# Kernel optimization log

Measured on AMD Instinct MI355X. Metric: run time of the kernel, lower is better.

Reference implementation:

```python
import jax, jax.numpy as jnp
import numpy as np
import math

NUM_HEADS = 16
NUM_BUCKETS = 32
MAX_DISTANCE = 128


def _relative_position_bucket(relative_position, num_buckets=NUM_BUCKETS, max_distance=MAX_DISTANCE):
    num_buckets = num_buckets // 2
    ret = (relative_position >= 0).astype(jnp.int32) * num_buckets
    n = jnp.abs(relative_position)
    max_exact = num_buckets // 2
    is_small = n < max_exact
    # guard log(0); masked by is_small anyway
    n_safe = jnp.maximum(n, 1).astype(jnp.float32)
    val_if_large = max_exact + (
        jnp.log(n_safe / max_exact) / math.log(max_distance / max_exact) * (num_buckets - max_exact)
    ).astype(jnp.int32)
    val_if_large = jnp.minimum(val_if_large, num_buckets - 1)
    return ret + jnp.where(is_small, n, val_if_large)


def compute_bias(rel_bias, query_length, key_length):
    ctx = jnp.arange(query_length)[:, None]
    mem = jnp.arange(key_length)[None, :]
    rp = mem - ctx  # [Q, K]
    bucket = _relative_position_bucket(rp)  # [Q, K]
    values = rel_bias[bucket]  # [Q, K, H]
    return jnp.transpose(values, (2, 0, 1))[None]  # [1, H, Q, K]


def setup_inputs() -> dict:
    key = jax.random.key(0)
    ks = jax.random.split(key, 6)
    B, S, D = 2, 2048, 1024
    sd = 1.0 / math.sqrt(D)
    return {
        "x": jax.random.normal(ks[0], (B, S, D), jnp.float32),
        "wq": jax.random.normal(ks[1], (D, D), jnp.float32) * sd,
        "wk": jax.random.normal(ks[2], (D, D), jnp.float32) * sd,
        "wv": jax.random.normal(ks[3], (D, D), jnp.float32) * sd,
        "wo": jax.random.normal(ks[4], (D, D), jnp.float32) * sd,
        "rel_bias": jax.random.normal(ks[5], (NUM_BUCKETS, NUM_HEADS), jnp.float32),
    }


def reference(x, wq, wk, wv, wo, rel_bias):
    B, S, _ = x.shape
    inner_dim = wq.shape[0]
    head_dim = inner_dim // NUM_HEADS
    # nn.Linear stores weight as [out, in]: y = x @ W^T
    q = (x @ wq.T).reshape(B, S, NUM_HEADS, head_dim).transpose(0, 2, 1, 3)
    k = (x @ wk.T).reshape(B, S, NUM_HEADS, head_dim).transpose(0, 2, 1, 3)
    v = (x @ wv.T).reshape(B, S, NUM_HEADS, head_dim).transpose(0, 2, 1, 3)
    scores = jnp.einsum('bhqd,bhkd->bhqk', q, k) / math.sqrt(head_dim)
    past_bias = compute_bias(rel_bias, S, S)  # [1, H, S, S]
    scores = scores + past_bias
    attn_weights = jax.nn.softmax(scores, axis=-1)
    attn_output = jnp.einsum('bhqk,bhkd->bhqd', attn_weights, v)
    attn_output = attn_output.transpose(0, 2, 1, 3).reshape(B, S, inner_dim)
    attn_output = attn_output @ wo.T
    return (attn_output, past_bias)
```

## Files before the change

### kernel.cpp

```cpp
#include <hip/hip_runtime.h>

typedef __bf16 bf16_t;
typedef __bf16 bf16x8 __attribute__((ext_vector_type(8)));
typedef float  f32x4  __attribute__((ext_vector_type(4)));
typedef float  f32x4u __attribute__((ext_vector_type(4), aligned(4)));

#define ASYNC16(g, l) __builtin_amdgcn_global_load_lds( \
    (const __attribute__((address_space(1))) void*)(g), \
    (__attribute__((address_space(3))) void*)(l), 16, 0, 0)

#define MFMA(a, b, c) __builtin_amdgcn_mfma_f32_16x16x32_bf16(a, b, c, 0, 0, 0)

__global__ __launch_bounds__(256) void cast_all(
    const float* __restrict__ x, const float* __restrict__ wq,
    const float* __restrict__ wk, const float* __restrict__ wv,
    const float* __restrict__ wo,
    bf16_t* __restrict__ xb, bf16_t* __restrict__ wqkvb, bf16_t* __restrict__ wob)
{
  int i4 = blockIdx.x * 256 + threadIdx.x;
  int base = i4 * 4;
  const float* src; bf16_t* dst;
  if (base < 4194304) { src = x + base; dst = xb + base; }
  else {
    int j = base - 4194304;
    int w = j >> 20, o = j & 1048575;
    if      (w == 0) { src = wq + o; dst = wqkvb + o; }
    else if (w == 1) { src = wk + o; dst = wqkvb + (1 << 20) + o; }
    else if (w == 2) { src = wv + o; dst = wqkvb + (2 << 20) + o; }
    else             { src = wo + o; dst = wob + o; }
  }
  float4 v = *(const float4*)src;
  union { bf16_t h[4]; uint2 u; } pk;
  pk.h[0] = (bf16_t)v.x; pk.h[1] = (bf16_t)v.y;
  pk.h[2] = (bf16_t)v.z; pk.h[3] = (bf16_t)v.w;
  *(uint2*)dst = pk.u;
}

__global__ void build_tbl(const float* __restrict__ rel_bias,
                          float* __restrict__ tblB, float* __restrict__ tblE)
{
  int i = blockIdx.x * 256 + threadIdx.x;
  if (i >= 4095 * 16) return;
  int rpi = i >> 4;
  int h = i & 15;
  int rp = rpi - 2047;
  int ret = rp >= 0 ? 16 : 0;
  int n = rp < 0 ? -rp : rp;
  int b;
  if (n < 8) b = ret + n;
  else {
    double v = 2.0 * (log2((double)n) - 3.0);
    int bi = 8 + (int)v;
    b = ret + (bi < 15 ? bi : 15);
  }
  float v = rel_bias[b * 16 + h];
  tblB[h * 4096 + rpi] = v;
  tblE[h * 4096 + rpi] = v * 1.4426950408889634f;
}

__global__ __launch_bounds__(256) void gemm_qkv(
    const bf16_t* __restrict__ A, const bf16_t* __restrict__ B,
    bf16_t* __restrict__ qk, bf16_t* __restrict__ vt)
{
  const int K = 1024;
  __shared__ bf16_t As[128 * 32];
  __shared__ bf16_t Bs[128 * 32];
  const int t = threadIdx.x;
  const int w = t >> 6, l = t & 63, ln = l & 15, quad = l >> 4;
  const int wm = (w & 1) * 64, wn = (w >> 1) * 64;
  const int m0 = blockIdx.x * 128, n0 = blockIdx.y * 128;

  f32x4 acc[4][4] = {};
  const int rA = t >> 2, c8 = (t & 3) * 8;
  const bf16_t* Ag = A + (size_t)(m0 + rA) * K + c8;
  const bf16_t* Bg = B + (size_t)(n0 + rA) * K + c8;
  const size_t K64 = (size_t)64 * K;
  bf16_t* As0 = &As[t * 8];  bf16_t* As1 = &As[2048 + t * 8];
  bf16_t* Bs0 = &Bs[t * 8];  bf16_t* Bs1 = &Bs[2048 + t * 8];

  for (int kt = 0; kt < K; kt += 32) {
    ASYNC16(Ag + kt,       As0);
    ASYNC16(Ag + kt + K64, As1);
    ASYNC16(Bg + kt,       Bs0);
    ASYNC16(Bg + kt + K64, Bs1);
    __syncthreads();
    bf16x8 a[4], b[4];
#pragma unroll
    for (int mi = 0; mi < 4; ++mi)
      a[mi] = *(const bf16x8*)&As[(wm + mi * 16 + ln) * 32 + quad * 8];
#pragma unroll
    for (int ni = 0; ni < 4; ++ni)
      b[ni] = *(const bf16x8*)&Bs[(wn + ni * 16 + ln) * 32 + quad * 8];
#pragma unroll
    for (int mi = 0; mi < 4; ++mi)
#pragma unroll
      for (int ni = 0; ni < 4; ++ni)
        acc[mi][ni] = MFMA(a[mi], b[ni], acc[mi][ni]);
    __syncthreads();
  }

  if (n0 >= 2048) {
#pragma unroll
    for (int mi = 0; mi < 4; ++mi)
#pragma unroll
      for (int ni = 0; ni < 4; ++ni) {
        int col = n0 + wn + ni * 16 + ln - 2048;
        int hh = col >> 6, dd = col & 63;
        int row = m0 + wm + mi * 16 + quad * 4;
        int bb = row >> 11, ss = row & 2047;
        union { bf16_t h4[4]; uint2 u; } pk;
#pragma unroll
        for (int j = 0; j < 4; ++j) pk.h4[j] = (bf16_t)acc[mi][ni][j];
        *(uint2*)&vt[((size_t)(bb * 16 + hh) * 64 + dd) * 2048 + ss] = pk.u;
      }
  } else {
#pragma unroll
    for (int mi = 0; mi < 4; ++mi)
#pragma unroll
      for (int ni = 0; ni < 4; ++ni) {
        int row = m0 + wm + mi * 16 + quad * 4;
        int col = n0 + wn + ni * 16 + ln;
#pragma unroll
        for (int j = 0; j < 4; ++j)
          qk[(size_t)(row + j) * 2048 + col] = (bf16_t)acc[mi][ni][j];
      }
  }
}

__global__ __launch_bounds__(256) void gemm_wo(
    const bf16_t* __restrict__ A, const bf16_t* __restrict__ B,
    float* __restrict__ C)
{
  const int K = 1024, N = 1024;
  __shared__ bf16_t As[64 * 32];
  __shared__ bf16_t Bs[128 * 32];
  const int t = threadIdx.x;
  const int w = t >> 6, l = t & 63, ln = l & 15, quad = l >> 4;
  const int wm = (w & 1) * 32, wn = (w >> 1) * 64;
  const int m0 = blockIdx.x * 64, n0 = blockIdx.y * 128;

  f32x4 acc[2][4] = {};
  const int rr = t >> 2, c8 = (t & 3) * 8;
  const bf16_t* Ag = A + (size_t)(m0 + rr) * K + c8;
  const bf16_t* Bg = B + (size_t)(n0 + rr) * K + c8;
  const size_t K64 = (size_t)64 * K;
  bf16_t* As0 = &As[t * 8];
  bf16_t* Bs0 = &Bs[t * 8];  bf16_t* Bs1 = &Bs[2048 + t * 8];

  for (int kt = 0; kt < K; kt += 32) {
    ASYNC16(Ag + kt,       As0);
    ASYNC16(Bg + kt,       Bs0);
    ASYNC16(Bg + kt + K64, Bs1);
    __syncthreads();
    bf16x8 a[2], b[4];
#pragma unroll
    for (int mi = 0; mi < 2; ++mi)
      a[mi] = *(const bf16x8*)&As[(wm + mi * 16 + ln) * 32 + quad * 8];
#pragma unroll
    for (int ni = 0; ni < 4; ++ni)
      b[ni] = *(const bf16x8*)&Bs[(wn + ni * 16 + ln) * 32 + quad * 8];
#pragma unroll
    for (int mi = 0; mi < 2; ++mi)
#pragma unroll
      for (int ni = 0; ni < 4; ++ni)
        acc[mi][ni] = MFMA(a[mi], b[ni], acc[mi][ni]);
    __syncthreads();
  }

#pragma unroll
  for (int mi = 0; mi < 2; ++mi)
#pragma unroll
    for (int ni = 0; ni < 4; ++ni) {
      int row = m0 + wm + mi * 16 + quad * 4;
      int col = n0 + wn + ni * 16 + ln;
#pragma unroll
      for (int j = 0; j < 4; ++j)
        C[(size_t)(row + j) * N + col] = acc[mi][ni][j];
    }
}

__global__ __launch_bounds__(512, 4) void flash_attn(
    const bf16_t* __restrict__ qk, const bf16_t* __restrict__ vt,
    const float* __restrict__ tblE, bf16_t* __restrict__ attn)
{
  __shared__ __align__(16) bf16_t Kt[128 * 64];
  __shared__ __align__(16) bf16_t Vs[64 * 128];
  __shared__ __align__(16) bf16_t Ps[8 * 16 * 128];
  const int t = threadIdx.x, w = t >> 6, l = t & 63, ln = l & 15, quad = l >> 4;
  const int q0 = blockIdx.x * 128, h = blockIdx.y, b = blockIdx.z;
  const int S = 2048;
  const int q = q0 + w * 16 + ln;

  const bf16_t* Qp = qk + (size_t)(b * S + q) * 2048 + h * 64 + quad * 8;
  bf16x8 bq0 = *(const bf16x8*)Qp;
  bf16x8 bq1 = *(const bf16x8*)(Qp + 32);

  f32x4 o[4] = {};
  float li = 0.f;

  const int krow = l >> 3;
  const int kg8  = ((l & 7) ^ krow) * 8;
  const int vrow = l >> 4;
  const int vg8  = ((l & 15) ^ ((w & 3) * 4 + vrow)) * 8;
  const bf16_t* Kg = qk + (size_t)(b * S) * 2048 + 1024 + h * 64 + kg8;
  const bf16_t* Vg = vt + (size_t)(b * 16 + h) * 64 * 2048 + vg8;
  const float* tb = tblE + h * 4096 + 2047 - q;

  for (int kt = 0; kt < S; kt += 128) {
    __syncthreads();
    ASYNC16(Kg + (size_t)(kt + w * 8 + krow) * 2048,      &Kt[(w * 8) * 64 + l * 8]);
    ASYNC16(Kg + (size_t)(kt + 64 + w * 8 + krow) * 2048, &Kt[(64 + w * 8) * 64 + l * 8]);
    ASYNC16(Vg + (size_t)(w * 4 + vrow) * 2048 + kt,      &Vs[(w * 4) * 128 + l * 8]);
    ASYNC16(Vg + (size_t)(32 + w * 4 + vrow) * 2048 + kt, &Vs[(32 + w * 4) * 128 + l * 8]);
    __syncthreads();

    const float* tbk = tb + kt;
    bf16_t* pw = &Ps[w * 2048 + ln * 128];
#pragma unroll
    for (int f = 0; f < 8; ++f) {
      const bf16_t* kp = &Kt[(f * 16 + ln) * 64];
      bf16x8 a0 = *(const bf16x8*)(kp + ((quad ^ (ln & 7)) * 8));
      bf16x8 a1 = *(const bf16x8*)(kp + (((4 + quad) ^ (ln & 7)) * 8));
      f32x4 acc = {};
      acc = MFMA(a0, bq0, acc);
      acc = MFMA(a1, bq1, acc);
      f32x4u bv = *(const f32x4u*)(tbk + f * 16 + quad * 4);
      union { bf16_t h4[4]; uint2 u; } pk;
#pragma unroll
      for (int j = 0; j < 4; ++j) {
        float p = __builtin_amdgcn_exp2f(fmaf(acc[j], 0.18033688011112042f, bv[j]));
        li += p;
        pk.h4[j] = (bf16_t)p;
      }
      *(uint2*)&pw[(((2 * f + (quad >> 1)) ^ ln) * 8) + (quad & 1) * 4] = pk.u;
    }

#pragma unroll
    for (int kk = 0; kk < 4; ++kk) {
      bf16x8 bp = *(const bf16x8*)&Ps[w * 2048 + ln * 128 + (((kk * 4 + quad) ^ ln) * 8)];
#pragma unroll
      for (int dt = 0; dt < 4; ++dt) {
        bf16x8 av = *(const bf16x8*)&Vs[(dt * 16 + ln) * 128 + (((kk * 4 + quad) ^ ln) * 8)];
        o[dt] = MFMA(av, bp, o[dt]);
      }
    }
  }

  li += __shfl_xor(li, 16);
  li += __shfl_xor(li, 32);
  float inv = 1.f / li;
  bf16_t* op = attn + (size_t)(b * S + q) * 1024 + h * 64 + quad * 4;
#pragma unroll
  for (int dt = 0; dt < 4; ++dt) {
    union { bf16_t h4[4]; uint2 u; } pk;
#pragma unroll
    for (int j = 0; j < 4; ++j) pk.h4[j] = (bf16_t)(o[dt][j] * inv);
    *(uint2*)&op[dt * 16] = pk.u;
  }
}

__global__ __launch_bounds__(256) void bias_out(const float* __restrict__ tbl,
                                                float* __restrict__ out1)
{
  int i = blockIdx.x * 256 + threadIdx.x;
  int hq = i >> 9;
  int k4 = (i & 511) * 4;
  int h = hq >> 11, q = hq & 2047;
  const float* tp = tbl + (h << 12) + (k4 - q + 2047);
  float4 v;
  v.x = __ldg(tp);     v.y = __ldg(tp + 1);
  v.z = __ldg(tp + 2); v.w = __ldg(tp + 3);
  ((float4*)out1)[i] = v;
}

extern "C" void kernel_launch(void* const* d_in, const int* in_sizes, int n_in,
                              void* d_out, int out_size, void* d_ws, size_t ws_size,
                              hipStream_t stream)
{
  const float* x  = (const float*)d_in[0];
  const float* wq = (const float*)d_in[1];
  const float* wk = (const float*)d_in[2];
  const float* wv = (const float*)d_in[3];
  const float* wo = (const float*)d_in[4];
  const float* rb = (const float*)d_in[5];
  float* out0 = (float*)d_out;
  float* out1 = out0 + 4194304;

  char* ws = (char*)d_ws;
  bf16_t* xb    = (bf16_t*)(ws);
  bf16_t* wqkvb = (bf16_t*)(ws + 8388608);
  bf16_t* wob   = (bf16_t*)(ws + 14680064);
  bf16_t* qk    = (bf16_t*)(ws + 16777216);
  bf16_t* vt    = (bf16_t*)(ws + 33554432);
  float*  tblB  = (float*)(ws + 41943040);
  float*  tblE  = (float*)(ws + 42205184);
  bf16_t* attnb = xb;

  cast_all<<<8192, 256, 0, stream>>>(x, wq, wk, wv, wo, xb, wqkvb, wob);
  build_tbl<<<256, 256, 0, stream>>>(rb, tblB, tblE);
  gemm_qkv<<<dim3(32, 24), 256, 0, stream>>>(xb, wqkvb, qk, vt);
  flash_attn<<<dim3(16, 16, 2), 512, 0, stream>>>(qk, vt, tblE, attnb);
  gemm_wo<<<dim3(64, 8), 256, 0, stream>>>(attnb, wob, out0);
  bias_out<<<65536, 256, 0, stream>>>(tblB, out1);
}
```

Baseline: 410.8 us.

## Process two query tiles per wave in flash attention, halving block threads

Each wave of the attention kernel now handles 32 query rows, as two 16-row sub-tiles, instead of 16, so the block drops from 512 to 256 threads. Each K fragment and V fragment read from LDS is reused for two MFMAs. The cost being targeted is LDS read traffic per MFMA. In exchange, register pressure roughly doubles for the accumulators, launch bounds drop to 2 blocks per CU, and there is less latency hiding from wave count.

```diff
diff --git a/kernel.cpp b/kernel.cpp
--- a/kernel.cpp
+++ b/kernel.cpp
@@ -179,83 +179,109 @@
     }
 }
 
-__global__ __launch_bounds__(512, 4) void flash_attn(
+__global__ __launch_bounds__(256, 2) void flash_attn(
     const bf16_t* __restrict__ qk, const bf16_t* __restrict__ vt,
     const float* __restrict__ tblE, bf16_t* __restrict__ attn)
 {
   __shared__ __align__(16) bf16_t Kt[128 * 64];
   __shared__ __align__(16) bf16_t Vs[64 * 128];
-  __shared__ __align__(16) bf16_t Ps[8 * 16 * 128];
+  __shared__ __align__(16) bf16_t Ps[4 * 32 * 128];
   const int t = threadIdx.x, w = t >> 6, l = t & 63, ln = l & 15, quad = l >> 4;
   const int q0 = blockIdx.x * 128, h = blockIdx.y, b = blockIdx.z;
   const int S = 2048;
-  const int q = q0 + w * 16 + ln;
-
-  const bf16_t* Qp = qk + (size_t)(b * S + q) * 2048 + h * 64 + quad * 8;
-  bf16x8 bq0 = *(const bf16x8*)Qp;
-  bf16x8 bq1 = *(const bf16x8*)(Qp + 32);
-
-  f32x4 o[4] = {};
-  float li = 0.f;
+  const int qa = q0 + w * 32 + ln;
+  const int qb = qa + 16;
+
+  const bf16_t* Qpa = qk + (size_t)(b * S + qa) * 2048 + h * 64 + quad * 8;
+  const bf16_t* Qpb = qk + (size_t)(b * S + qb) * 2048 + h * 64 + quad * 8;
+  bf16x8 bq0a = *(const bf16x8*)Qpa;
+  bf16x8 bq1a = *(const bf16x8*)(Qpa + 32);
+  bf16x8 bq0b = *(const bf16x8*)Qpb;
+  bf16x8 bq1b = *(const bf16x8*)(Qpb + 32);
+
+  f32x4 oa[4] = {}, ob[4] = {};
+  float lia = 0.f, lib = 0.f;
 
   const int krow = l >> 3;
   const int kg8  = ((l & 7) ^ krow) * 8;
   const int vrow = l >> 4;
-  const int vg8  = ((l & 15) ^ ((w & 3) * 4 + vrow)) * 8;
+  const int vg8  = ((l & 15) ^ (w * 4 + vrow)) * 8;
   const bf16_t* Kg = qk + (size_t)(b * S) * 2048 + 1024 + h * 64 + kg8;
   const bf16_t* Vg = vt + (size_t)(b * 16 + h) * 64 * 2048 + vg8;
-  const float* tb = tblE + h * 4096 + 2047 - q;
+  const float* tba = tblE + h * 4096 + 2047 - qa;
+  const float* tbb = tblE + h * 4096 + 2047 - qb;
 
   for (int kt = 0; kt < S; kt += 128) {
     __syncthreads();
-    ASYNC16(Kg + (size_t)(kt + w * 8 + krow) * 2048,      &Kt[(w * 8) * 64 + l * 8]);
-    ASYNC16(Kg + (size_t)(kt + 64 + w * 8 + krow) * 2048, &Kt[(64 + w * 8) * 64 + l * 8]);
-    ASYNC16(Vg + (size_t)(w * 4 + vrow) * 2048 + kt,      &Vs[(w * 4) * 128 + l * 8]);
-    ASYNC16(Vg + (size_t)(32 + w * 4 + vrow) * 2048 + kt, &Vs[(32 + w * 4) * 128 + l * 8]);
-    __syncthreads();
-
-    const float* tbk = tb + kt;
-    bf16_t* pw = &Ps[w * 2048 + ln * 128];
+#pragma unroll
+    for (int cc = 0; cc < 4; ++cc) {
+      int kr0 = w * 8 + cc * 32;
+      ASYNC16(Kg + (size_t)(kt + kr0 + krow) * 2048, &Kt[kr0 * 64 + l * 8]);
+      int vr0 = w * 4 + cc * 16;
+      ASYNC16(Vg + (size_t)(vr0 + vrow) * 2048 + kt, &Vs[vr0 * 128 + l * 8]);
+    }
+    __syncthreads();
+
+    const float* tbka = tba + kt;
+    const float* tbkb = tbb + kt;
+    bf16_t* pwa = &Ps[w * 4096 + ln * 128];
+    bf16_t* pwb = pwa + 16 * 128;
 #pragma unroll
     for (int f = 0; f < 8; ++f) {
       const bf16_t* kp = &Kt[(f * 16 + ln) * 64];
       bf16x8 a0 = *(const bf16x8*)(kp + ((quad ^ (ln & 7)) * 8));
       bf16x8 a1 = *(const bf16x8*)(kp + (((4 + quad) ^ (ln & 7)) * 8));
-      f32x4 acc = {};
-      acc = MFMA(a0, bq0, acc);
-      acc = MFMA(a1, bq1, acc);
-      f32x4u bv = *(const f32x4u*)(tbk + f * 16 + quad * 4);
-      union { bf16_t h4[4]; uint2 u; } pk;
+      f32x4 acca = {}, accb = {};
+      acca = MFMA(a0, bq0a, acca);
+      acca = MFMA(a1, bq1a, acca);
+      accb = MFMA(a0, bq0b, accb);
+      accb = MFMA(a1, bq1b, accb);
+      f32x4u bva = *(const f32x4u*)(tbka + f * 16 + quad * 4);
+      f32x4u bvb = *(const f32x4u*)(tbkb + f * 16 + quad * 4);
+      union { bf16_t h4[4]; uint2 u; } pka, pkb;
 #pragma unroll
       for (int j = 0; j < 4; ++j) {
-        float p = __builtin_amdgcn_exp2f(fmaf(acc[j], 0.18033688011112042f, bv[j]));
-        li += p;
-        pk.h4[j] = (bf16_t)p;
+        float pa = __builtin_amdgcn_exp2f(fmaf(acca[j], 0.18033688011112042f, bva[j]));
+        float pb = __builtin_amdgcn_exp2f(fmaf(accb[j], 0.18033688011112042f, bvb[j]));
+        lia += pa; lib += pb;
+        pka.h4[j] = (bf16_t)pa; pkb.h4[j] = (bf16_t)pb;
       }
-      *(uint2*)&pw[(((2 * f + (quad >> 1)) ^ ln) * 8) + (quad & 1) * 4] = pk.u;
+      int po = (((2 * f + (quad >> 1)) ^ ln) * 8) + (quad & 1) * 4;
+      *(uint2*)&pwa[po] = pka.u;
+      *(uint2*)&pwb[po] = pkb.u;
     }
 
 #pragma unroll
     for (int kk = 0; kk < 4; ++kk) {
-      bf16x8 bp = *(const bf16x8*)&Ps[w * 2048 + ln * 128 + (((kk * 4 + quad) ^ ln) * 8)];
+      int so = ((kk * 4 + quad) ^ ln) * 8;
+      bf16x8 bpa = *(const bf16x8*)&pwa[so];
+      bf16x8 bpb = *(const bf16x8*)&pwb[so];
 #pragma unroll
       for (int dt = 0; dt < 4; ++dt) {
-        bf16x8 av = *(const bf16x8*)&Vs[(dt * 16 + ln) * 128 + (((kk * 4 + quad) ^ ln) * 8)];
-        o[dt] = MFMA(av, bp, o[dt]);
+        bf16x8 av = *(const bf16x8*)&Vs[(dt * 16 + ln) * 128 + so];
+        oa[dt] = MFMA(av, bpa, oa[dt]);
+        ob[dt] = MFMA(av, bpb, ob[dt]);
       }
     }
   }
 
-  li += __shfl_xor(li, 16);
-  li += __shfl_xor(li, 32);
-  float inv = 1.f / li;
-  bf16_t* op = attn + (size_t)(b * S + q) * 1024 + h * 64 + quad * 4;
+  lia += __shfl_xor(lia, 16);
+  lia += __shfl_xor(lia, 32);
+  lib += __shfl_xor(lib, 16);
+  lib += __shfl_xor(lib, 32);
+  float inva = 1.f / lia, invb = 1.f / lib;
+  bf16_t* opa = attn + (size_t)(b * S + qa) * 1024 + h * 64 + quad * 4;
+  bf16_t* opb = attn + (size_t)(b * S + qb) * 1024 + h * 64 + quad * 4;
 #pragma unroll
   for (int dt = 0; dt < 4; ++dt) {
-    union { bf16_t h4[4]; uint2 u; } pk;
-#pragma unroll
-    for (int j = 0; j < 4; ++j) pk.h4[j] = (bf16_t)(o[dt][j] * inv);
-    *(uint2*)&op[dt * 16] = pk.u;
+    union { bf16_t h4[4]; uint2 u; } pka, pkb;
+#pragma unroll
+    for (int j = 0; j < 4; ++j) {
+      pka.h4[j] = (bf16_t)(oa[dt][j] * inva);
+      pkb.h4[j] = (bf16_t)(ob[dt][j] * invb);
+    }
+    *(uint2*)&opa[dt * 16] = pka.u;
+    *(uint2*)&opb[dt * 16] = pkb.u;
   }
 }
 
@@ -299,7 +325,7 @@
   cast_all<<<8192, 256, 0, stream>>>(x, wq, wk, wv, wo, xb, wqkvb, wob);
   build_tbl<<<256, 256, 0, stream>>>(rb, tblB, tblE);
   gemm_qkv<<<dim3(32, 24), 256, 0, stream>>>(xb, wqkvb, qk, vt);
-  flash_attn<<<dim3(16, 16, 2), 512, 0, stream>>>(qk, vt, tblE, attnb);
+  flash_attn<<<dim3(16, 16, 2), 256, 0, stream>>>(qk, vt, tblE, attnb);
   gemm_wo<<<dim3(64, 8), 256, 0, stream>>>(attnb, wob, out0);
   bias_out<<<65536, 256, 0, stream>>>(tblB, out1);
 }
```

Measured after the change: 408.9 us. Within noise of the previous version (-0.5%).
